# Kernel optimization log

Measured on AMD Instinct MI355X. Metric: run time of the kernel, lower is better.

Reference implementation:

```python
import jax, jax.numpy as jnp
import numpy as np

N = 100000
E = 3200000
F_IN, H1, H2, C = 128, 64, 32, 10


def setup_inputs() -> dict:
    key = jax.random.key(0)
    ks = jax.random.split(key, 8)
    x = jax.random.normal(ks[0], (N, F_IN), dtype=jnp.float32)
    edge_index = jax.random.randint(ks[1], (2, E), 0, N, dtype=jnp.int64)
    W1 = jax.random.normal(ks[2], (F_IN, H1), dtype=jnp.float32) / np.sqrt(F_IN)
    b1 = jnp.zeros((H1,), dtype=jnp.float32)
    W2 = jax.random.normal(ks[3], (H1, H2), dtype=jnp.float32) / np.sqrt(H1)
    b2 = jnp.zeros((H2,), dtype=jnp.float32)
    Wc = jax.random.normal(ks[4], (H2, C), dtype=jnp.float32) / np.sqrt(H2)
    bc = jnp.zeros((C,), dtype=jnp.float32)
    return {"x": x, "edge_index": edge_index, "W1": W1, "b1": b1,
            "W2": W2, "b2": b2, "Wc": Wc, "bc": bc}


def gcn_conv(x, src, dst, W, b, n):
    # PyG GCNConv: x' = D^{-1/2} (A + I) D^{-1/2} (X W) + b
    h = x @ W                                        # [N, H]
    ones = jnp.ones((src.shape[0],), dtype=h.dtype)
    deg = jax.ops.segment_sum(ones, dst, num_segments=n) + 1.0  # +1 self loop
    dinv = jax.lax.rsqrt(deg)                        # deg >= 1, safe
    norm = dinv[src] * dinv[dst]                     # [E]
    msg = h[src] * norm[:, None]                     # [E, H] gather + scale
    agg = jax.ops.segment_sum(msg, dst, num_segments=n)
    # self-loop contribution: norm_ii = 1/deg_i
    out = agg + h * (dinv * dinv)[:, None]
    return out + b


def reference(x, edge_index, W1, b1, W2, b2, Wc, bc):
    n = x.shape[0]
    src, dst = edge_index[0], edge_index[1]
    h = gcn_conv(x, src, dst, W1, b1, n)
    h = jax.nn.relu(h)
    # dropout is identity in eval mode (training=False)
    h = gcn_conv(h, src, dst, W2, b2, n)
    h = jax.nn.relu(h)
    logits = h @ Wc + bc
    return jax.nn.log_softmax(logits, axis=1)
```

## Files before the change

### kernel.cpp

```cpp
#include <hip/hip_runtime.h>


#define BSHIFT 8
#define BMASK 255
#define NBUCK_MAX 512
#define TILE 4096
#define EPT 16
#define NPW 4

__device__ __forceinline__ unsigned pack_bf16(float lo, float hi) {
    unsigned ul = __float_as_uint(lo);
    ul = (ul + 0x7FFFu + ((ul >> 16) & 1u)) >> 16;
    unsigned uh = __float_as_uint(hi);
    uh = ((uh + 0x7FFFu + ((uh >> 16) & 1u)) >> 16) << 16;
    return ul | uh;
}

__global__ void k_hist(const int* __restrict__ dst, int* __restrict__ bcnt, int E) {
    __shared__ int h[NBUCK_MAX];
    for (int i = threadIdx.x; i < NBUCK_MAX; i += blockDim.x) h[i] = 0;
    __syncthreads();
    for (int e = blockIdx.x * blockDim.x + threadIdx.x; e < E; e += gridDim.x * blockDim.x)
        atomicAdd(&h[dst[e] >> BSHIFT], 1);
    __syncthreads();
    for (int i = threadIdx.x; i < NBUCK_MAX; i += blockDim.x)
        if (h[i]) atomicAdd(&bcnt[i], h[i]);
}

__global__ void k_scanb(const int* __restrict__ bcnt, int* __restrict__ bbase,
                        int* __restrict__ gcur, int E) {
    __shared__ int s[NBUCK_MAX];
    int t = threadIdx.x;
    int v = bcnt[t];
    s[t] = v;
    __syncthreads();
    for (int o = 1; o < NBUCK_MAX; o <<= 1) {
        int u = (t >= o) ? s[t - o] : 0;
        __syncthreads();
        s[t] += u;
        __syncthreads();
    }
    int ex = s[t] - v;
    bbase[t] = ex;
    gcur[t] = ex;
    if (t == NBUCK_MAX - 1) bbase[NBUCK_MAX] = E;
}

__global__ __launch_bounds__(256) void k_binA(const int* __restrict__ src,
                                              const int* __restrict__ dst,
                                              int* __restrict__ gcur,
                                              int* __restrict__ binned, int E) {
    __shared__ int hist[NBUCK_MAX];
    __shared__ int lbase[NBUCK_MAX];
    __shared__ int gdelta[NBUCK_MAX];
    __shared__ int cnt2[NBUCK_MAX];
    __shared__ int scanb[256];
    __shared__ int stage[TILE];
    __shared__ unsigned short sbucket[TILE];

    int t = threadIdx.x;
    for (int i = t; i < NBUCK_MAX; i += 256) { hist[i] = 0; cnt2[i] = 0; }
    __syncthreads();

    int tileStart = blockIdx.x * TILE;
    int cntTile = min(TILE, E - tileStart);

    int vals[EPT];
    int bks[EPT];
#pragma unroll
    for (int i = 0; i < EPT; i++) {
        int e = tileStart + t + i * 256;
        if (e < E) {
            int s = src[e], d = dst[e];
            vals[i] = s | ((d & BMASK) << 17);
            bks[i] = d >> BSHIFT;
            atomicAdd(&hist[bks[i]], 1);
        } else bks[i] = -1;
    }
    __syncthreads();

    int a0 = hist[2 * t], a1 = hist[2 * t + 1];
    int ts = a0 + a1;
    scanb[t] = ts;
    __syncthreads();
    for (int o = 1; o < 256; o <<= 1) {
        int u = (t >= o) ? scanb[t - o] : 0;
        __syncthreads();
        scanb[t] += u;
        __syncthreads();
    }
    int ex = scanb[t] - ts;
    lbase[2 * t] = ex;
    lbase[2 * t + 1] = ex + a0;
    __syncthreads();

    for (int b = t; b < NBUCK_MAX; b += 256) {
        int c = hist[b];
        int g = c ? atomicAdd(&gcur[b], c) : 0;
        gdelta[b] = g - lbase[b];
    }
#pragma unroll
    for (int i = 0; i < EPT; i++) {
        if (bks[i] >= 0) {
            int rr = atomicAdd(&cnt2[bks[i]], 1);
            int slot = lbase[bks[i]] + rr;
            stage[slot] = vals[i];
            sbucket[slot] = (unsigned short)bks[i];
        }
    }
    __syncthreads();
    for (int i = t; i < cntTile; i += 256) {
        int b = sbucket[i];
        binned[gdelta[b] + i] = stage[i];
    }
}

__global__ void k_sortcsr(const int* __restrict__ bbase, const int* __restrict__ binned,
                          int* __restrict__ rowptr, float* __restrict__ dinv,
                          int* __restrict__ csr, int n, int E) {
    __shared__ int cnt[256];
    __shared__ int sc[256];
    __shared__ int rpl[256];
    __shared__ int lcur[256];
    int b = blockIdx.x, t = threadIdx.x;
    cnt[t] = 0; lcur[t] = 0;
    __syncthreads();
    int beg = bbase[b], end = bbase[b + 1];
    for (int i = beg + t; i < end; i += 256)
        atomicAdd(&cnt[(binned[i] >> 17) & BMASK], 1);
    __syncthreads();
    int v = cnt[t];
    sc[t] = v;
    __syncthreads();
    for (int o = 1; o < 256; o <<= 1) {
        int u = (t >= o) ? sc[t - o] : 0;
        __syncthreads();
        sc[t] += u;
        __syncthreads();
    }
    int rp = beg + sc[t] - v;
    rpl[t] = rp;
    int g = (b << BSHIFT) + t;
    if (g < n) {
        rowptr[g] = rp;
        dinv[g] = rsqrtf((float)v + 1.0f);
        if (g == n - 1) rowptr[n] = E;
    }
    __syncthreads();
    for (int i = beg + t; i < end; i += 256) {
        int vv = binned[i];
        int ln = (vv >> 17) & BMASK;
        int k = atomicAdd(&lcur[ln], 1);
        csr[rpl[ln] + k] = vv & 0x1FFFF;
    }
}

template<int K, int M, int R>
__global__ __launch_bounds__(256) void k_gemm(const float* __restrict__ X,
                                              const float* __restrict__ W,
                                              const float* __restrict__ dinv,
                                              unsigned* __restrict__ hsb, int n) {
    constexpr int MW = M / 4;
    __shared__ float Ws[K * M];
    for (int i = threadIdx.x; i < K * M; i += 256) Ws[i] = W[i];
    __syncthreads();
    int w = threadIdx.x >> 6, lane = threadIdx.x & 63;
    int wo = w * MW;
    int r0 = blockIdx.x * (64 * R) + lane;
    float acc[R][MW];
#pragma unroll
    for (int i = 0; i < R; i++)
#pragma unroll
        for (int j = 0; j < MW; j++) acc[i][j] = 0.f;

    for (int k = 0; k < K; k += 4) {
        float4 xv[R];
#pragma unroll
        for (int i = 0; i < R; i++) {
            int rr = r0 + 64 * i;
            xv[i] = (rr < n) ? *(const float4*)(X + (size_t)rr * K + k)
                             : make_float4(0.f, 0.f, 0.f, 0.f);
        }
#pragma unroll
        for (int kk = 0; kk < 4; kk++) {
#pragma unroll
            for (int j = 0; j < MW; j += 4) {
                float4 wv = *(const float4*)&Ws[(k + kk) * M + wo + j];
#pragma unroll
                for (int i = 0; i < R; i++) {
                    float xs = (kk == 0) ? xv[i].x : (kk == 1) ? xv[i].y
                             : (kk == 2) ? xv[i].z : xv[i].w;
                    acc[i][j + 0] += xs * wv.x;
                    acc[i][j + 1] += xs * wv.y;
                    acc[i][j + 2] += xs * wv.z;
                    acc[i][j + 3] += xs * wv.w;
                }
            }
        }
    }
#pragma unroll
    for (int i = 0; i < R; i++) {
        int rr = r0 + 64 * i;
        if (rr < n) {
            float di = dinv[rr];
            unsigned p[MW / 2];
#pragma unroll
            for (int jj = 0; jj < MW / 2; jj++)
                p[jj] = pack_bf16(acc[i][2 * jj] * di, acc[i][2 * jj + 1] * di);
            unsigned* hr = hsb + (size_t)rr * (M / 2) + wo / 2;
#pragma unroll
            for (int jj = 0; jj < MW / 2; jj += 4)
                *(uint4*)(hr + jj) = make_uint4(p[jj], p[jj + 1], p[jj + 2], p[jj + 3]);
        }
    }
}

#define ACC8(V) \
    acc[0] += __uint_as_float((V).x << 16);  acc[1] += __uint_as_float((V).x & 0xFFFF0000u); \
    acc[2] += __uint_as_float((V).y << 16);  acc[3] += __uint_as_float((V).y & 0xFFFF0000u); \
    acc[4] += __uint_as_float((V).z << 16);  acc[5] += __uint_as_float((V).z & 0xFFFF0000u); \
    acc[6] += __uint_as_float((V).w << 16);  acc[7] += __uint_as_float((V).w & 0xFFFF0000u);

__global__ __launch_bounds__(256) void k_agg64f(
        const int* __restrict__ rowptr, const int* __restrict__ csr,
        const uint4* __restrict__ hsb, const float* __restrict__ dinv,
        const float* __restrict__ b1, const float* __restrict__ W2,
        unsigned* __restrict__ hsb2, int n) {
    int wid = (blockIdx.x * blockDim.x + threadIdx.x) >> 6;
    int lane = threadIdx.x & 63;
    int q = lane >> 3, r = lane & 7;
    int d0 = wid * NPW;
    if (d0 >= n) return;
    float w2r[8][4];
    float b1r[8];
#pragma unroll
    for (int i = 0; i < 8; i++) {
        b1r[i] = b1[8 * r + i];
#pragma unroll
        for (int jj = 0; jj < 4; jj++)
            w2r[i][jj] = W2[(8 * r + i) * 32 + 4 * q + jj];
    }
    int dend = min(d0 + NPW, n);
    int rp = rowptr[min(d0 + min(lane, NPW), n)];
    int beg = __shfl(rp, 0, 64);
    int end = __shfl(rp, 1, 64);
    int cc = min(end - beg, 64);
    int idxv = (lane < cc) ? csr[beg + lane] : 0;
    for (int d = d0; d < dend; d++) {
        int kk = d - d0;
        int nbeg = __shfl(rp, min(kk + 1, NPW), 64);
        int nend = __shfl(rp, min(kk + 2, NPW), 64);
        int ncc = min(nend - nbeg, 64);
        int nidxv = 0;
        if (d + 1 < dend) nidxv = (lane < ncc) ? csr[nbeg + lane] : 0;
        uint4 wsf = hsb[(size_t)d * 8 + r];
        float di = dinv[d];
        float acc[8];
#pragma unroll
        for (int i = 0; i < 8; i++) acc[i] = 0.f;
        int j = 0;
        for (; j + 16 <= cc; j += 16) {
            int sA = __shfl(idxv, j + q, 64);
            int sB = __shfl(idxv, j + 8 + q, 64);
            uint4 wA = hsb[(size_t)sA * 8 + r];
            uint4 wB = hsb[(size_t)sB * 8 + r];
            ACC8(wA)
            ACC8(wB)
        }
        {
            int tA = j + q, tB = j + 8 + q;
            int sA = __shfl(idxv, tA & 63, 64);
            int sB = __shfl(idxv, tB & 63, 64);
            if (tA < cc) { uint4 wv = hsb[(size_t)sA * 8 + r]; ACC8(wv) }
            if (tB < cc) { uint4 wv = hsb[(size_t)sB * 8 + r]; ACC8(wv) }
        }
        for (int c = beg + 64; c < end; c += 16) {
            if (c + q < end)     { uint4 wv = hsb[(size_t)csr[c + q] * 8 + r]; ACC8(wv) }
            if (c + 8 + q < end) { uint4 wv = hsb[(size_t)csr[c + 8 + q] * 8 + r]; ACC8(wv) }
        }
#pragma unroll
        for (int i = 0; i < 8; i++) {
            acc[i] += __shfl_xor(acc[i], 8, 64);
            acc[i] += __shfl_xor(acc[i], 16, 64);
            acc[i] += __shfl_xor(acc[i], 32, 64);
        }
        ACC8(wsf)
        float v[8];
#pragma unroll
        for (int i = 0; i < 8; i++) v[i] = fmaxf(acc[i] * di + b1r[i], 0.f);
        float h[4] = {0.f, 0.f, 0.f, 0.f};
#pragma unroll
        for (int i = 0; i < 8; i++)
#pragma unroll
            for (int jj = 0; jj < 4; jj++) h[jj] += v[i] * w2r[i][jj];
#pragma unroll
        for (int jj = 0; jj < 4; jj++) {
            h[jj] += __shfl_xor(h[jj], 1, 64);
            h[jj] += __shfl_xor(h[jj], 2, 64);
            h[jj] += __shfl_xor(h[jj], 4, 64);
        }
        if (r == 0) {
            unsigned p0 = pack_bf16(h[0] * di, h[1] * di);
            unsigned p1 = pack_bf16(h[2] * di, h[3] * di);
            *(uint2*)(hsb2 + (size_t)d * 16 + 2 * q) = make_uint2(p0, p1);
        }
        beg = nbeg; end = nend; cc = ncc; idxv = nidxv;
    }
}

__global__ __launch_bounds__(256) void k_agg32f(
        const int* __restrict__ rowptr, const int* __restrict__ csr,
        const uint4* __restrict__ hsb2, const float* __restrict__ dinv,
        const float* __restrict__ b2, const float* __restrict__ Wc,
        const float* __restrict__ bc, float* __restrict__ out, int n) {
    int wid = (blockIdx.x * blockDim.x + threadIdx.x) >> 6;
    int lane = threadIdx.x & 63;
    int q = lane >> 2, r = lane & 3;
    int d0 = wid * NPW;
    if (d0 >= n) return;
    float wcr[8];
    float b2r[8];
    float bcr = (q < 10) ? bc[q] : 0.f;
#pragma unroll
    for (int i = 0; i < 8; i++) {
        b2r[i] = b2[8 * r + i];
        wcr[i] = (q < 10) ? Wc[(8 * r + i) * 10 + q] : 0.f;
    }
    int dend = min(d0 + NPW, n);
    int rp = rowptr[min(d0 + min(lane, NPW), n)];
    int beg = __shfl(rp, 0, 64);
    int end = __shfl(rp, 1, 64);
    int cc = min(end - beg, 64);
    int idxv = (lane < cc) ? csr[beg + lane] : 0;
    for (int d = d0; d < dend; d++) {
        int kk = d - d0;
        int nbeg = __shfl(rp, min(kk + 1, NPW), 64);
        int nend = __shfl(rp, min(kk + 2, NPW), 64);
        int ncc = min(nend - nbeg, 64);
        int nidxv = 0;
        if (d + 1 < dend) nidxv = (lane < ncc) ? csr[nbeg + lane] : 0;
        uint4 wsf = hsb2[(size_t)d * 4 + r];
        float di = dinv[d];
        float acc[8];
#pragma unroll
        for (int i = 0; i < 8; i++) acc[i] = 0.f;
        int j = 0;
        for (; j + 32 <= cc; j += 32) {
            int sA = __shfl(idxv, j + q, 64);
            int sB = __shfl(idxv, j + 16 + q, 64);
            uint4 wA = hsb2[(size_t)sA * 4 + r];
            uint4 wB = hsb2[(size_t)sB * 4 + r];
            ACC8(wA)
            ACC8(wB)
        }
        {
            int tA = j + q, tB = j + 16 + q;
            int sA = __shfl(idxv, tA & 63, 64);
            int sB = __shfl(idxv, tB & 63, 64);
            if (tA < cc) { uint4 wv = hsb2[(size_t)sA * 4 + r]; ACC8(wv) }
            if (tB < cc) { uint4 wv = hsb2[(size_t)sB * 4 + r]; ACC8(wv) }
        }
        for (int c = beg + 64; c < end; c += 32) {
            if (c + q < end)      { uint4 wv = hsb2[(size_t)csr[c + q] * 4 + r]; ACC8(wv) }
            if (c + 16 + q < end) { uint4 wv = hsb2[(size_t)csr[c + 16 + q] * 4 + r]; ACC8(wv) }
        }
#pragma unroll
        for (int i = 0; i < 8; i++) {
            acc[i] += __shfl_xor(acc[i], 4, 64);
            acc[i] += __shfl_xor(acc[i], 8, 64);
            acc[i] += __shfl_xor(acc[i], 16, 64);
            acc[i] += __shfl_xor(acc[i], 32, 64);
        }
        ACC8(wsf)
        float part = 0.f;
#pragma unroll
        for (int i = 0; i < 8; i++) {
            float v = fmaxf(acc[i] * di + b2r[i], 0.f);
            part += v * wcr[i];
        }
        part += __shfl_xor(part, 1, 64);
        part += __shfl_xor(part, 2, 64);
        float mylogit = part + bcr;
        float m = -1e30f;
        float l[10];
#pragma unroll
        for (int c = 0; c < 10; c++) {
            l[c] = __shfl(mylogit, 4 * c, 64);
            m = fmaxf(m, l[c]);
        }
        float ssum = 0.f;
#pragma unroll
        for (int c = 0; c < 10; c++) ssum += __expf(l[c] - m);
        float lse = m + __logf(ssum);
        if (r == 0 && q < 10) out[(size_t)d * 10 + q] = mylogit - lse;
        beg = nbeg; end = nend; cc = ncc; idxv = nidxv;
    }
}

extern "C" void kernel_launch(void* const* d_in, const int* in_sizes, int n_in,
                              void* d_out, int out_size, void* d_ws, size_t ws_size,
                              hipStream_t stream) {
    const float* x  = (const float*)d_in[0];
    const int*   ei = (const int*)d_in[1];
    const float* W1 = (const float*)d_in[2];
    const float* b1 = (const float*)d_in[3];
    const float* W2 = (const float*)d_in[4];
    const float* b2 = (const float*)d_in[5];
    const float* Wc = (const float*)d_in[6];
    const float* bc = (const float*)d_in[7];
    float* out = (float*)d_out;

    const int N = in_sizes[0] / 128;
    const int E = in_sizes[1] / 2;
    const int* src = ei;
    const int* dst = ei + E;

    const int NBUCK = (N + BMASK) >> BSHIFT;
    const int NTILE = (E + TILE - 1) / TILE;
    const int NW = (N + NPW - 1) / NPW;

    char* ws = (char*)d_ws;
    size_t off = 0;
    auto alloc = [&](size_t elems) {
        void* p = ws + off;
        off += ((elems * 4 + 1023) & ~(size_t)1023);
        return p;
    };
    float*    dinv   = (float*)alloc(N);
    int*      bcnt   = (int*)alloc(NBUCK_MAX);
    int*      bbase  = (int*)alloc(NBUCK_MAX + 1);
    int*      gcur   = (int*)alloc(NBUCK_MAX);
    int*      rowptr = (int*)alloc(N + 1);
    int*      binned = (int*)alloc(E);
    int*      csr    = (int*)alloc(E);
    unsigned* hsb    = (unsigned*)alloc((size_t)N * 32);
    unsigned* hsb2   = (unsigned*)alloc((size_t)N * 16);

    hipMemsetAsync(bcnt, 0, sizeof(int) * NBUCK_MAX, stream);

    k_hist<<<512, 256, 0, stream>>>(dst, bcnt, E);
    k_scanb<<<1, NBUCK_MAX, 0, stream>>>(bcnt, bbase, gcur, E);
    k_binA<<<NTILE, 256, 0, stream>>>(src, dst, gcur, binned, E);
    k_sortcsr<<<NBUCK, 256, 0, stream>>>(bbase, binned, rowptr, dinv, csr, N, E);

    k_gemm<128, 64, 2><<<(N + 127) / 128, 256, 0, stream>>>(x, W1, dinv, hsb, N);
    k_agg64f<<<(NW * 64 + 255) / 256, 256, 0, stream>>>(rowptr, csr, (const uint4*)hsb,
                                                        dinv, b1, W2, hsb2, N);
    k_agg32f<<<(NW * 64 + 255) / 256, 256, 0, stream>>>(rowptr, csr, (const uint4*)hsb2,
                                                        dinv, b2, Wc, bc, out, N);
}
```

Measured before the change: 363.3 us.

## Replace bucketed two-pass CSR build with global-atomic count, scan, and scatter

Swaps the shared-memory bucket binning and per-bucket local sort for a plain CSR build: global atomic degree count, a three-kernel prefix scan, and an atomic-cursor scatter of sources into CSR. This drops the intermediate binned array and the bucket-sort kernels. In exchange it uses 3.2M global atomics twice on random addresses, and neighbour order within each row becomes nondeterministic. That order affects the floating-point summation order, and it may hurt locality in the scatter writes.

New measurement: 685.2 us. 88.6% more time.

```diff
diff --git a/kernel.cpp b/kernel.cpp
--- a/kernel.cpp
+++ b/kernel.cpp
@@ -1,11 +1,6 @@
 #include <hip/hip_runtime.h>
 
 
-#define BSHIFT 8
-#define BMASK 255
-#define NBUCK_MAX 512
-#define TILE 4096
-#define EPT 16
 #define NPW 4
 
 __device__ __forceinline__ unsigned pack_bf16(float lo, float hi) {
@@ -16,144 +11,75 @@
     return ul | uh;
 }
 
-__global__ void k_hist(const int* __restrict__ dst, int* __restrict__ bcnt, int E) {
-    __shared__ int h[NBUCK_MAX];
-    for (int i = threadIdx.x; i < NBUCK_MAX; i += blockDim.x) h[i] = 0;
-    __syncthreads();
-    for (int e = blockIdx.x * blockDim.x + threadIdx.x; e < E; e += gridDim.x * blockDim.x)
-        atomicAdd(&h[dst[e] >> BSHIFT], 1);
-    __syncthreads();
-    for (int i = threadIdx.x; i < NBUCK_MAX; i += blockDim.x)
-        if (h[i]) atomicAdd(&bcnt[i], h[i]);
-}
-
-__global__ void k_scanb(const int* __restrict__ bcnt, int* __restrict__ bbase,
-                        int* __restrict__ gcur, int E) {
-    __shared__ int s[NBUCK_MAX];
+
+__global__ __launch_bounds__(256) void k_count(const int* __restrict__ dst,
+                                               int* __restrict__ deg, int E) {
+    int e = blockIdx.x * 256 + threadIdx.x;
+    if (e < E) atomicAdd(&deg[dst[e]], 1);
+}
+
+__global__ __launch_bounds__(256) void k_scanA(const int* __restrict__ deg,
+                                               int* __restrict__ lscan,
+                                               int* __restrict__ bsum, int n) {
+    __shared__ int s[256];
     int t = threadIdx.x;
-    int v = bcnt[t];
+    int i = blockIdx.x * 256 + t;
+    int v = (i < n) ? deg[i] : 0;
     s[t] = v;
     __syncthreads();
-    for (int o = 1; o < NBUCK_MAX; o <<= 1) {
+    for (int o = 1; o < 256; o <<= 1) {
         int u = (t >= o) ? s[t - o] : 0;
         __syncthreads();
         s[t] += u;
         __syncthreads();
     }
-    int ex = s[t] - v;
-    bbase[t] = ex;
-    gcur[t] = ex;
-    if (t == NBUCK_MAX - 1) bbase[NBUCK_MAX] = E;
-}
-
-__global__ __launch_bounds__(256) void k_binA(const int* __restrict__ src,
-                                              const int* __restrict__ dst,
-                                              int* __restrict__ gcur,
-                                              int* __restrict__ binned, int E) {
-    __shared__ int hist[NBUCK_MAX];
-    __shared__ int lbase[NBUCK_MAX];
-    __shared__ int gdelta[NBUCK_MAX];
-    __shared__ int cnt2[NBUCK_MAX];
-    __shared__ int scanb[256];
-    __shared__ int stage[TILE];
-    __shared__ unsigned short sbucket[TILE];
-
+    if (i < n) lscan[i] = s[t] - v;
+    if (t == 255) bsum[blockIdx.x] = s[255];
+}
+
+__global__ void k_scanB(const int* __restrict__ bsum, int* __restrict__ bbase, int nb) {
+    __shared__ int s[512];
     int t = threadIdx.x;
-    for (int i = t; i < NBUCK_MAX; i += 256) { hist[i] = 0; cnt2[i] = 0; }
+    int v = (t < nb) ? bsum[t] : 0;
+    s[t] = v;
     __syncthreads();
-
-    int tileStart = blockIdx.x * TILE;
-    int cntTile = min(TILE, E - tileStart);
-
-    int vals[EPT];
-    int bks[EPT];
-#pragma unroll
-    for (int i = 0; i < EPT; i++) {
-        int e = tileStart + t + i * 256;
-        if (e < E) {
-            int s = src[e], d = dst[e];
-            vals[i] = s | ((d & BMASK) << 17);
-            bks[i] = d >> BSHIFT;
-            atomicAdd(&hist[bks[i]], 1);
-        } else bks[i] = -1;
-    }
-    __syncthreads();
-
-    int a0 = hist[2 * t], a1 = hist[2 * t + 1];
-    int ts = a0 + a1;
-    scanb[t] = ts;
-    __syncthreads();
-    for (int o = 1; o < 256; o <<= 1) {
-        int u = (t >= o) ? scanb[t - o] : 0;
+    for (int o = 1; o < 512; o <<= 1) {
+        int u = (t >= o) ? s[t - o] : 0;
         __syncthreads();
-        scanb[t] += u;
+        s[t] += u;
         __syncthreads();
     }
-    int ex = scanb[t] - ts;
-    lbase[2 * t] = ex;
-    lbase[2 * t + 1] = ex + a0;
-    __syncthreads();
-
-    for (int b = t; b < NBUCK_MAX; b += 256) {
-        int c = hist[b];
-        int g = c ? atomicAdd(&gcur[b], c) : 0;
-        gdelta[b] = g - lbase[b];
-    }
-#pragma unroll
-    for (int i = 0; i < EPT; i++) {
-        if (bks[i] >= 0) {
-            int rr = atomicAdd(&cnt2[bks[i]], 1);
-            int slot = lbase[bks[i]] + rr;
-            stage[slot] = vals[i];
-            sbucket[slot] = (unsigned short)bks[i];
-        }
-    }
-    __syncthreads();
-    for (int i = t; i < cntTile; i += 256) {
-        int b = sbucket[i];
-        binned[gdelta[b] + i] = stage[i];
-    }
-}
-
-__global__ void k_sortcsr(const int* __restrict__ bbase, const int* __restrict__ binned,
-                          int* __restrict__ rowptr, float* __restrict__ dinv,
-                          int* __restrict__ csr, int n, int E) {
-    __shared__ int cnt[256];
-    __shared__ int sc[256];
-    __shared__ int rpl[256];
-    __shared__ int lcur[256];
-    int b = blockIdx.x, t = threadIdx.x;
-    cnt[t] = 0; lcur[t] = 0;
-    __syncthreads();
-    int beg = bbase[b], end = bbase[b + 1];
-    for (int i = beg + t; i < end; i += 256)
-        atomicAdd(&cnt[(binned[i] >> 17) & BMASK], 1);
-    __syncthreads();
-    int v = cnt[t];
-    sc[t] = v;
-    __syncthreads();
-    for (int o = 1; o < 256; o <<= 1) {
-        int u = (t >= o) ? sc[t - o] : 0;
-        __syncthreads();
-        sc[t] += u;
-        __syncthreads();
-    }
-    int rp = beg + sc[t] - v;
-    rpl[t] = rp;
-    int g = (b << BSHIFT) + t;
-    if (g < n) {
-        rowptr[g] = rp;
-        dinv[g] = rsqrtf((float)v + 1.0f);
-        if (g == n - 1) rowptr[n] = E;
-    }
-    __syncthreads();
-    for (int i = beg + t; i < end; i += 256) {
-        int vv = binned[i];
-        int ln = (vv >> 17) & BMASK;
-        int k = atomicAdd(&lcur[ln], 1);
-        csr[rpl[ln] + k] = vv & 0x1FFFF;
-    }
-}
+    if (t < nb) bbase[t] = s[t] - v;
+}
+
+__global__ __launch_bounds__(256) void k_scanC(const int* __restrict__ deg,
+                                               const int* __restrict__ lscan,
+                                               const int* __restrict__ bbase,
+                                               int* __restrict__ rowptr,
+                                               int* __restrict__ cur,
+                                               float* __restrict__ dinv, int n, int E) {
+    int i = blockIdx.x * 256 + threadIdx.x;
+    if (i < n) {
+        int rp = lscan[i] + bbase[blockIdx.x];
+        rowptr[i] = rp;
+        cur[i] = rp;
+        dinv[i] = rsqrtf((float)deg[i] + 1.0f);
+        if (i == n - 1) rowptr[n] = E;
+    }
+}
+
+__global__ __launch_bounds__(256) void k_place(const int* __restrict__ src,
+                                               const int* __restrict__ dst,
+                                               int* __restrict__ cur,
+                                               int* __restrict__ csr, int E) {
+    int e = blockIdx.x * 256 + threadIdx.x;
+    if (e < E) {
+        int d = dst[e];
+        int p = atomicAdd(&cur[d], 1);
+        csr[p] = src[e];
+    }
+}
+
 
 template<int K, int M, int R>
 __global__ __launch_bounds__(256) void k_gemm(const float* __restrict__ X,
@@ -415,8 +341,8 @@
     const int* src = ei;
     const int* dst = ei + E;
 
-    const int NBUCK = (N + BMASK) >> BSHIFT;
-    const int NTILE = (E + TILE - 1) / TILE;
+    const int NB = (N + 255) / 256;
+    const int NEB = (E + 255) / 256;
     const int NW = (N + NPW - 1) / NPW;
 
     char* ws = (char*)d_ws;
@@ -427,21 +353,23 @@
         return p;
     };
     float*    dinv   = (float*)alloc(N);
-    int*      bcnt   = (int*)alloc(NBUCK_MAX);
-    int*      bbase  = (int*)alloc(NBUCK_MAX + 1);
-    int*      gcur   = (int*)alloc(NBUCK_MAX);
     int*      rowptr = (int*)alloc(N + 1);
-    int*      binned = (int*)alloc(E);
+    int*      deg    = (int*)alloc(N);
+    int*      lscan  = (int*)alloc(N);
+    int*      cur    = (int*)alloc(N);
+    int*      bsum   = (int*)alloc(512);
+    int*      bbase  = (int*)alloc(512);
     int*      csr    = (int*)alloc(E);
     unsigned* hsb    = (unsigned*)alloc((size_t)N * 32);
     unsigned* hsb2   = (unsigned*)alloc((size_t)N * 16);
 
-    hipMemsetAsync(bcnt, 0, sizeof(int) * NBUCK_MAX, stream);
-
-    k_hist<<<512, 256, 0, stream>>>(dst, bcnt, E);
-    k_scanb<<<1, NBUCK_MAX, 0, stream>>>(bcnt, bbase, gcur, E);
-    k_binA<<<NTILE, 256, 0, stream>>>(src, dst, gcur, binned, E);
-    k_sortcsr<<<NBUCK, 256, 0, stream>>>(bbase, binned, rowptr, dinv, csr, N, E);
+    hipMemsetAsync(deg, 0, sizeof(int) * N, stream);
+
+    k_count<<<NEB, 256, 0, stream>>>(dst, deg, E);
+    k_scanA<<<NB, 256, 0, stream>>>(deg, lscan, bsum, N);
+    k_scanB<<<1, 512, 0, stream>>>(bsum, bbase, NB);
+    k_scanC<<<NB, 256, 0, stream>>>(deg, lscan, bbase, rowptr, cur, dinv, N, E);
+    k_place<<<NEB, 256, 0, stream>>>(src, dst, cur, csr, E);
 
     k_gemm<128, 64, 2><<<(N + 127) / 128, 256, 0, stream>>>(x, W1, dinv, hsb, N);
     k_agg64f<<<(NW * 64 + 255) / 256, 256, 0, stream>>>(rowptr, csr, (const uint4*)hsb,
```

## Fold bucket scan into binning kernels and stage CSR writes in LDS

Applied to the files above, without the earlier changes.

Removes the separate single-block scan kernel by having each k_binA and k_sortcsr block recompute the bucket prefix sum from the histogram counts. Global write cursors become zero-initialised offsets added to that base, and one memset now clears both arrays because they sit next to each other in the workspace. k_sortcsr also scatters its CSR entries into a 48KB LDS staging buffer and then writes them out contiguously, replacing random global stores. In exchange, every block repeats a redundant 512-entry scan, and the larger LDS footprint may lower occupancy in k_sortcsr.

Result: no change. 359.6 us (median of 2 runs) (-1.0%).

```diff
diff --git a/kernel.cpp b/kernel.cpp
--- a/kernel.cpp
+++ b/kernel.cpp
@@ -7,6 +7,7 @@
 #define TILE 4096
 #define EPT 16
 #define NPW 4
+#define SCAP 12288
 
 __device__ __forceinline__ unsigned pack_bf16(float lo, float hi) {
     unsigned ul = __float_as_uint(lo);
@@ -27,39 +28,36 @@
         if (h[i]) atomicAdd(&bcnt[i], h[i]);
 }
 
-__global__ void k_scanb(const int* __restrict__ bcnt, int* __restrict__ bbase,
-                        int* __restrict__ gcur, int E) {
-    __shared__ int s[NBUCK_MAX];
-    int t = threadIdx.x;
-    int v = bcnt[t];
-    s[t] = v;
-    __syncthreads();
-    for (int o = 1; o < NBUCK_MAX; o <<= 1) {
-        int u = (t >= o) ? s[t - o] : 0;
-        __syncthreads();
-        s[t] += u;
-        __syncthreads();
-    }
-    int ex = s[t] - v;
-    bbase[t] = ex;
-    gcur[t] = ex;
-    if (t == NBUCK_MAX - 1) bbase[NBUCK_MAX] = E;
-}
-
 __global__ __launch_bounds__(256) void k_binA(const int* __restrict__ src,
                                               const int* __restrict__ dst,
-                                              int* __restrict__ gcur,
+                                              const int* __restrict__ bcnt,
+                                              int* __restrict__ gcur0,
                                               int* __restrict__ binned, int E) {
     __shared__ int hist[NBUCK_MAX];
     __shared__ int lbase[NBUCK_MAX];
+    __shared__ int gbase[NBUCK_MAX];
     __shared__ int gdelta[NBUCK_MAX];
     __shared__ int cnt2[NBUCK_MAX];
     __shared__ int scanb[256];
+    __shared__ int scanc[256];
     __shared__ int stage[TILE];
     __shared__ unsigned short sbucket[TILE];
 
     int t = threadIdx.x;
     for (int i = t; i < NBUCK_MAX; i += 256) { hist[i] = 0; cnt2[i] = 0; }
+    int c0 = bcnt[2 * t], c1 = bcnt[2 * t + 1];
+    int cs = c0 + c1;
+    scanc[t] = cs;
+    __syncthreads();
+    for (int o = 1; o < 256; o <<= 1) {
+        int u = (t >= o) ? scanc[t - o] : 0;
+        __syncthreads();
+        scanc[t] += u;
+        __syncthreads();
+    }
+    int ex2 = scanc[t] - cs;
+    gbase[2 * t] = ex2;
+    gbase[2 * t + 1] = ex2 + c0;
     __syncthreads();
 
     int tileStart = blockIdx.x * TILE;
@@ -96,7 +94,7 @@
 
     for (int b = t; b < NBUCK_MAX; b += 256) {
         int c = hist[b];
-        int g = c ? atomicAdd(&gcur[b], c) : 0;
+        int g = c ? (gbase[b] + atomicAdd(&gcur0[b], c)) : 0;
         gdelta[b] = g - lbase[b];
     }
 #pragma unroll
@@ -115,17 +113,37 @@
     }
 }
 
-__global__ void k_sortcsr(const int* __restrict__ bbase, const int* __restrict__ binned,
-                          int* __restrict__ rowptr, float* __restrict__ dinv,
-                          int* __restrict__ csr, int n, int E) {
+__global__ __launch_bounds__(256) void k_sortcsr(const int* __restrict__ bcnt,
+                                                 const int* __restrict__ binned,
+                                                 int* __restrict__ rowptr,
+                                                 float* __restrict__ dinv,
+                                                 int* __restrict__ csr, int n, int E) {
     __shared__ int cnt[256];
     __shared__ int sc[256];
     __shared__ int rpl[256];
     __shared__ int lcur[256];
+    __shared__ int gbase[NBUCK_MAX];
+    __shared__ int scanc[256];
+    __shared__ int stage2[SCAP];
     int b = blockIdx.x, t = threadIdx.x;
     cnt[t] = 0; lcur[t] = 0;
-    __syncthreads();
-    int beg = bbase[b], end = bbase[b + 1];
+    int c0 = bcnt[2 * t], c1 = bcnt[2 * t + 1];
+    int cs = c0 + c1;
+    scanc[t] = cs;
+    __syncthreads();
+    for (int o = 1; o < 256; o <<= 1) {
+        int u = (t >= o) ? scanc[t - o] : 0;
+        __syncthreads();
+        scanc[t] += u;
+        __syncthreads();
+    }
+    int ex2 = scanc[t] - cs;
+    gbase[2 * t] = ex2;
+    gbase[2 * t + 1] = ex2 + c0;
+    __syncthreads();
+
+    int beg = gbase[b];
+    int end = (b + 1 < NBUCK_MAX) ? gbase[b + 1] : E;
     for (int i = beg + t; i < end; i += 256)
         atomicAdd(&cnt[(binned[i] >> 17) & BMASK], 1);
     __syncthreads();
@@ -151,8 +169,14 @@
         int vv = binned[i];
         int ln = (vv >> 17) & BMASK;
         int k = atomicAdd(&lcur[ln], 1);
-        csr[rpl[ln] + k] = vv & 0x1FFFF;
-    }
+        int idx = rpl[ln] + k - beg;
+        if (idx < SCAP) stage2[idx] = vv & 0x1FFFF;
+        else            csr[beg + idx] = vv & 0x1FFFF;
+    }
+    __syncthreads();
+    int cc = end - beg;
+    for (int i = t; i < cc; i += 256)
+        if (i < SCAP) csr[beg + i] = stage2[i];
 }
 
 template<int K, int M, int R>
@@ -428,20 +452,18 @@
     };
     float*    dinv   = (float*)alloc(N);
     int*      bcnt   = (int*)alloc(NBUCK_MAX);
-    int*      bbase  = (int*)alloc(NBUCK_MAX + 1);
-    int*      gcur   = (int*)alloc(NBUCK_MAX);
+    int*      gcur0  = (int*)alloc(NBUCK_MAX);
     int*      rowptr = (int*)alloc(N + 1);
     int*      binned = (int*)alloc(E);
     int*      csr    = (int*)alloc(E);
     unsigned* hsb    = (unsigned*)alloc((size_t)N * 32);
     unsigned* hsb2   = (unsigned*)alloc((size_t)N * 16);
 
-    hipMemsetAsync(bcnt, 0, sizeof(int) * NBUCK_MAX, stream);
+    hipMemsetAsync(bcnt, 0, sizeof(int) * NBUCK_MAX * 2, stream);
 
     k_hist<<<512, 256, 0, stream>>>(dst, bcnt, E);
-    k_scanb<<<1, NBUCK_MAX, 0, stream>>>(bcnt, bbase, gcur, E);
-    k_binA<<<NTILE, 256, 0, stream>>>(src, dst, gcur, binned, E);
-    k_sortcsr<<<NBUCK, 256, 0, stream>>>(bbase, binned, rowptr, dinv, csr, N, E);
+    k_binA<<<NTILE, 256, 0, stream>>>(src, dst, bcnt, gcur0, binned, E);
+    k_sortcsr<<<NBUCK, 256, 0, stream>>>(bcnt, binned, rowptr, dinv, csr, N, E);
 
     k_gemm<128, 64, 2><<<(N + 127) / 128, 256, 0, stream>>>(x, W1, dinv, hsb, N);
     k_agg64f<<<(NW * 64 + 255) / 256, 256, 0, stream>>>(rowptr, csr, (const uint4*)hsb,
```
